# Performance work log

Hardware: AMD Instinct MI355X
Metric: run time of the kernel (lower is better)

## Reference

```python
import jax, jax.numpy as jnp
import numpy as np

P = 2    # padding
R = 2    # ref[0]: rows/cols gathered as conv channels
WP = 3   # ref[1]: conv kernel length along border


def setup_inputs() -> dict:
    key = jax.random.key(0)
    ks = jax.random.split(key, 8)
    B, C, H, W = 8, 128, 256, 256
    HID = 8
    x = jax.random.normal(ks[0], (B, C, H, W), dtype=jnp.float32)
    # stacked params for 4 border MLPs: order top, bottom, left, right
    w1 = jax.random.normal(ks[1], (4, HID, R, WP), dtype=jnp.float32) * 0.3
    b1 = jax.random.normal(ks[2], (4, HID), dtype=jnp.float32) * 0.1
    w2 = jax.random.normal(ks[3], (4, HID, HID), dtype=jnp.float32) * 0.3
    b2 = jax.random.normal(ks[4], (4, HID), dtype=jnp.float32) * 0.1
    w3 = jax.random.normal(ks[5], (4, 1, HID), dtype=jnp.float32) * 0.3
    b3 = jax.random.normal(ks[6], (4, 1), dtype=jnp.float32) * 0.1
    return {"x": x, "w1": w1, "b1": b1, "w2": w2, "b2": b2, "w3": w3, "b3": b3}


def _mlp(slab, w1, b1, w2, b2, w3, b3):
    # slab: (B, R, L, C) -- R gathered lines as channels, L border length, C image channels
    L = slab.shape[2]
    # valid conv along L with WP taps: windows (B, R, WP, L-WP+1, C)
    wins = jnp.stack([slab[:, :, k:L - WP + 1 + k, :] for k in range(WP)], axis=2)
    h = jax.nn.relu(jnp.einsum('brklc,hrk->bhlc', wins, w1) + b1[None, :, None, None])
    h = jax.nn.relu(jnp.einsum('bhlc,gh->bglc', h, w2) + b2[None, :, None, None])
    o = jax.nn.relu(jnp.einsum('bglc,og->bolc', h, w3) + b3[None, :, None, None])
    return o[:, 0]  # (B, L-2, C)


def reference(x, w1, b1, w2, b2, w3, b3):
    B, C, H, W = x.shape
    H2, W2 = H + 2 * P, W + 2 * P
    xp = jnp.zeros((B, C, H2, W2), x.dtype).at[:, :, P:H + P, P:W + P].set(x)
    for i in range(P):
        # top: gather rows [P-i, P-i+R), write row P-1-i, cols 1:W2-1
        top = _mlp(jnp.transpose(xp[:, :, P - i:P + R - i, :], (0, 2, 3, 1)),
                   w1[0], b1[0], w2[0], b2[0], w3[0], b3[0])  # (B, W2-2, C)
        xp = xp.at[:, :, P - 1 - i, 1:W2 - 1].set(jnp.transpose(top, (0, 2, 1)))
        # bottom
        bot = _mlp(jnp.transpose(xp[:, :, H2 - 1 - (R + P) + i:H2 - 1 - P + i, :], (0, 2, 3, 1)),
                   w1[1], b1[1], w2[1], b2[1], w3[1], b3[1])
        xp = xp.at[:, :, H + P + i, 1:W2 - 1].set(jnp.transpose(bot, (0, 2, 1)))
        # left: gather cols, transpose so cols act as channels
        lef = _mlp(jnp.transpose(xp[:, :, :, P - i:P + R - i], (0, 3, 2, 1)),
                   w1[2], b1[2], w2[2], b2[2], w3[2], b3[2])  # (B, H2-2, C)
        xp = xp.at[:, :, 1:H2 - 1, P - 1 - i].set(jnp.transpose(lef, (0, 2, 1)))
        # right
        rig = _mlp(jnp.transpose(xp[:, :, :, W2 - 1 - (R + P) + i:W2 - 1 - P + i], (0, 3, 2, 1)),
                   w1[3], b1[3], w2[3], b2[3], w3[3], b3[3])
        xp = xp.at[:, :, 1:H2 - 1, W + P + i].set(jnp.transpose(rig, (0, 2, 1)))
    return xp
```

## Files before the change

### kernel.cpp

```cpp
#include <hip/hip_runtime.h>


__device__ __forceinline__ int bmap(int r) { return r < 4 ? r : r - 251; }

__device__ __forceinline__ float mlp6(const float* __restrict__ v,
                                      const float* __restrict__ W1s,
                                      const float* __restrict__ B1s,
                                      const float* __restrict__ W2s,
                                      const float* __restrict__ B2s,
                                      const float* __restrict__ W3s,
                                      float b3s)
{
    float h1[8];
#pragma unroll
    for (int h = 0; h < 8; ++h) {
        float a = B1s[h];
#pragma unroll
        for (int q = 0; q < 6; ++q) a = fmaf(v[q], W1s[h * 6 + q], a);
        h1[h] = fmaxf(a, 0.f);
    }
    float h2[8];
#pragma unroll
    for (int g = 0; g < 8; ++g) {
        float a = B2s[g];
#pragma unroll
        for (int h = 0; h < 8; ++h) a = fmaf(h1[h], W2s[g * 8 + h], a);
        h2[g] = fmaxf(a, 0.f);
    }
    float o = b3s;
#pragma unroll
    for (int g = 0; g < 8; ++g) o = fmaf(h2[g], W3s[g], o);
    return fmaxf(o, 0.f);
}

__global__ __launch_bounds__(256) void border_kernel(
    const float* __restrict__ x,
    const float* __restrict__ w1, const float* __restrict__ b1,
    const float* __restrict__ w2, const float* __restrict__ b2,
    const float* __restrict__ w3, const float* __restrict__ b3,
    float* __restrict__ out)
{
    const int tid = threadIdx.x;
    const int bc  = blockIdx.x;
    const float* xs = x + (size_t)bc * 65536;
    float*       os = out + (size_t)bc * 67600;

    __shared__ float rowS[9][260];
    __shared__ float colS[9][260];
    __shared__ float W1[4][8][6];
    __shared__ float B1[4][8];
    __shared__ float W2[4][8][8];
    __shared__ float B2[4][8];
    __shared__ float W3[4][8];
    __shared__ float B3[4];

    for (int idx = tid; idx < 9 * 260; idx += 256) {
        (&rowS[0][0])[idx] = 0.f;
        (&colS[0][0])[idx] = 0.f;
    }
    for (int idx = tid; idx < 4 * 8 * 6; idx += 256) (&W1[0][0][0])[idx] = w1[idx];
    for (int idx = tid; idx < 4 * 8 * 8; idx += 256) (&W2[0][0][0])[idx] = w2[idx];
    if (tid < 32) {
        (&B1[0][0])[tid] = b1[tid];
        (&B2[0][0])[tid] = b2[tid];
        (&W3[0][0])[tid] = w3[tid];
    }
    if (tid < 4) B3[tid] = b3[tid];
    __syncthreads();

    for (int which = 0; which < 5; ++which) {
        int xr = which < 2 ? which : 251 + which;
        rowS[2 + which][2 + tid] = xs[xr * 256 + tid];
        colS[2 + which][2 + tid] = xs[tid * 256 + xr];
    }
    __syncthreads();

    for (int it = 0; it < 2; ++it) {
        for (int task = tid; task < 516; task += 256) {
            int s, j;
            int rin0, rin1, rout;
            if (task < 258) { s = 0; j = task + 1;       rin0 = 2 - it;   rin1 = 3 - it;   rout = 1 - it; }
            else            { s = 1; j = task - 258 + 1; rin0 = 255 + it; rin1 = 256 + it; rout = 258 + it; }
            int a0 = bmap(rin0), a1 = bmap(rin1);
            float v[6];
            v[0] = rowS[a0][j - 1]; v[1] = rowS[a0][j]; v[2] = rowS[a0][j + 1];
            v[3] = rowS[a1][j - 1]; v[4] = rowS[a1][j]; v[5] = rowS[a1][j + 1];
            float o = mlp6(v, &W1[s][0][0], B1[s], &W2[s][0][0], B2[s], W3[s], B3[s]);
            rowS[bmap(rout)][j] = o;
            if (j < 4 || j >= 255) colS[bmap(j)][rout] = o;
        }
        __syncthreads();
        for (int task = tid; task < 516; task += 256) {
            int s, r;
            int cin0, cin1, cout;
            if (task < 258) { s = 2; r = task + 1;       cin0 = 2 - it;   cin1 = 3 - it;   cout = 1 - it; }
            else            { s = 3; r = task - 258 + 1; cin0 = 255 + it; cin1 = 256 + it; cout = 258 + it; }
            int a0 = bmap(cin0), a1 = bmap(cin1);
            float v[6];
            v[0] = colS[a0][r - 1]; v[1] = colS[a0][r]; v[2] = colS[a0][r + 1];
            v[3] = colS[a1][r - 1]; v[4] = colS[a1][r]; v[5] = colS[a1][r + 1];
            float o = mlp6(v, &W1[s][0][0], B1[s], &W2[s][0][0], B2[s], W3[s], B3[s]);
            colS[bmap(cout)][r] = o;
            if (r < 4 || r >= 255) rowS[bmap(r)][cout] = o;
        }
        __syncthreads();
    }

    for (int idx = tid; idx < 4 * 260; idx += 256) {
        int w = idx / 260, cc = idx % 260;
        int rr = w < 2 ? w : 256 + w;
        os[(size_t)rr * 260 + cc] = rowS[bmap(rr)][cc];
    }
    for (int idx = tid; idx < 4 * 256; idx += 256) {
        int w = idx >> 8, r = (idx & 255) + 2;
        int cc = w < 2 ? w : 256 + w;
        os[(size_t)r * 260 + cc] = colS[bmap(cc)][r];
    }
}

__global__ __launch_bounds__(256) void copy_kernel(const float* __restrict__ x,
                                                   float* __restrict__ out)
{
    const int n2 = 8 * 128 * 256 * 128;
    int i = blockIdx.x * 256 + threadIdx.x;
    const int stride = gridDim.x * 256;
    for (; i < n2; i += stride) {
        int row = i >> 7;
        int pos = (i & 127) << 1;
        int bc  = row >> 8;
        int r   = row & 255;
        const float2 val = *(const float2*)(x + ((size_t)row << 8) + pos);
        *(float2*)(out + (size_t)bc * 67600 + (r + 2) * 260 + 2 + pos) = val;
    }
}

extern "C" void kernel_launch(void* const* d_in, const int* in_sizes, int n_in,
                              void* d_out, int out_size, void* d_ws, size_t ws_size,
                              hipStream_t stream)
{
    const float* x  = (const float*)d_in[0];
    const float* w1 = (const float*)d_in[1];
    const float* b1 = (const float*)d_in[2];
    const float* w2 = (const float*)d_in[3];
    const float* b2 = (const float*)d_in[4];
    const float* w3 = (const float*)d_in[5];
    const float* b3 = (const float*)d_in[6];
    float* out = (float*)d_out;

    copy_kernel<<<2048, 256, 0, stream>>>(x, out);
    border_kernel<<<1024, 256, 0, stream>>>(x, w1, b1, w2, b2, w3, b3, out);
}
```

Before: 140.8 us.

## Run border kernel first, then assemble interior rows with aligned float4 stores

The MLP weights are no longer staged in shared memory. Each border stage is templated on its MLP index so the compiler can turn the weights into uniform scalar loads. The kernels run in the opposite order: border_kernel writes the border first, then assemble_kernel writes every full output row with 16-byte-aligned float4 stores, reading back the border columns it overwrites. This is meant to replace the misaligned float2 interior stores with wider aligned ones, at the cost of extra reads of already-written border values and a dependency between the two kernels.

```diff
diff --git a/kernel.cpp b/kernel.cpp
--- a/kernel.cpp
+++ b/kernel.cpp
@@ -3,34 +3,86 @@
 
 __device__ __forceinline__ int bmap(int r) { return r < 4 ? r : r - 251; }
 
+template <int S>
 __device__ __forceinline__ float mlp6(const float* __restrict__ v,
-                                      const float* __restrict__ W1s,
-                                      const float* __restrict__ B1s,
-                                      const float* __restrict__ W2s,
-                                      const float* __restrict__ B2s,
-                                      const float* __restrict__ W3s,
-                                      float b3s)
+                                      const float* __restrict__ w1,
+                                      const float* __restrict__ b1,
+                                      const float* __restrict__ w2,
+                                      const float* __restrict__ b2,
+                                      const float* __restrict__ w3,
+                                      const float* __restrict__ b3)
 {
+    const float* __restrict__ W1 = w1 + S * 48;
+    const float* __restrict__ B1 = b1 + S * 8;
+    const float* __restrict__ W2 = w2 + S * 64;
+    const float* __restrict__ B2 = b2 + S * 8;
+    const float* __restrict__ W3 = w3 + S * 8;
+    const float  b3s = b3[S];
+
     float h1[8];
 #pragma unroll
     for (int h = 0; h < 8; ++h) {
-        float a = B1s[h];
+        float a = B1[h];
 #pragma unroll
-        for (int q = 0; q < 6; ++q) a = fmaf(v[q], W1s[h * 6 + q], a);
+        for (int q = 0; q < 6; ++q) a = fmaf(v[q], W1[h * 6 + q], a);
         h1[h] = fmaxf(a, 0.f);
     }
     float h2[8];
 #pragma unroll
     for (int g = 0; g < 8; ++g) {
-        float a = B2s[g];
+        float a = B2[g];
 #pragma unroll
-        for (int h = 0; h < 8; ++h) a = fmaf(h1[h], W2s[g * 8 + h], a);
+        for (int h = 0; h < 8; ++h) a = fmaf(h1[h], W2[g * 8 + h], a);
         h2[g] = fmaxf(a, 0.f);
     }
     float o = b3s;
 #pragma unroll
-    for (int g = 0; g < 8; ++g) o = fmaf(h2[g], W3s[g], o);
+    for (int g = 0; g < 8; ++g) o = fmaf(h2[g], W3[g], o);
     return fmaxf(o, 0.f);
+}
+
+template <int S>
+__device__ __forceinline__ void hstage(int it, int tid,
+                                       float (*rowS)[260], float (*colS)[260],
+                                       const float* __restrict__ w1, const float* __restrict__ b1,
+                                       const float* __restrict__ w2, const float* __restrict__ b2,
+                                       const float* __restrict__ w3, const float* __restrict__ b3)
+{
+    int rin0, rin1, rout;
+    if (S == 0) { rin0 = 2 - it;   rin1 = 3 - it;   rout = 1 - it;   }
+    else        { rin0 = 255 + it; rin1 = 256 + it; rout = 258 + it; }
+    const int a0 = bmap(rin0), a1 = bmap(rin1), ao = bmap(rout);
+    for (int j0 = tid; j0 < 258; j0 += 256) {
+        int j = j0 + 1;
+        float v[6];
+        v[0] = rowS[a0][j - 1]; v[1] = rowS[a0][j]; v[2] = rowS[a0][j + 1];
+        v[3] = rowS[a1][j - 1]; v[4] = rowS[a1][j]; v[5] = rowS[a1][j + 1];
+        float o = mlp6<S>(v, w1, b1, w2, b2, w3, b3);
+        rowS[ao][j] = o;
+        if (j < 4 || j >= 255) colS[bmap(j)][rout] = o;
+    }
+}
+
+template <int S>
+__device__ __forceinline__ void vstage(int it, int tid,
+                                       float (*rowS)[260], float (*colS)[260],
+                                       const float* __restrict__ w1, const float* __restrict__ b1,
+                                       const float* __restrict__ w2, const float* __restrict__ b2,
+                                       const float* __restrict__ w3, const float* __restrict__ b3)
+{
+    int cin0, cin1, cout;
+    if (S == 2) { cin0 = 2 - it;   cin1 = 3 - it;   cout = 1 - it;   }
+    else        { cin0 = 255 + it; cin1 = 256 + it; cout = 258 + it; }
+    const int a0 = bmap(cin0), a1 = bmap(cin1), ao = bmap(cout);
+    for (int r0 = tid; r0 < 258; r0 += 256) {
+        int r = r0 + 1;
+        float v[6];
+        v[0] = colS[a0][r - 1]; v[1] = colS[a0][r]; v[2] = colS[a0][r + 1];
+        v[3] = colS[a1][r - 1]; v[4] = colS[a1][r]; v[5] = colS[a1][r + 1];
+        float o = mlp6<S>(v, w1, b1, w2, b2, w3, b3);
+        colS[ao][r] = o;
+        if (r < 4 || r >= 255) rowS[bmap(r)][cout] = o;
+    }
 }
 
 __global__ __launch_bounds__(256) void border_kernel(
@@ -47,25 +99,11 @@
 
     __shared__ float rowS[9][260];
     __shared__ float colS[9][260];
-    __shared__ float W1[4][8][6];
-    __shared__ float B1[4][8];
-    __shared__ float W2[4][8][8];
-    __shared__ float B2[4][8];
-    __shared__ float W3[4][8];
-    __shared__ float B3[4];
 
     for (int idx = tid; idx < 9 * 260; idx += 256) {
         (&rowS[0][0])[idx] = 0.f;
         (&colS[0][0])[idx] = 0.f;
     }
-    for (int idx = tid; idx < 4 * 8 * 6; idx += 256) (&W1[0][0][0])[idx] = w1[idx];
-    for (int idx = tid; idx < 4 * 8 * 8; idx += 256) (&W2[0][0][0])[idx] = w2[idx];
-    if (tid < 32) {
-        (&B1[0][0])[tid] = b1[tid];
-        (&B2[0][0])[tid] = b2[tid];
-        (&W3[0][0])[tid] = w3[tid];
-    }
-    if (tid < 4) B3[tid] = b3[tid];
     __syncthreads();
 
     for (int which = 0; which < 5; ++which) {
@@ -76,33 +114,11 @@
     __syncthreads();
 
     for (int it = 0; it < 2; ++it) {
-        for (int task = tid; task < 516; task += 256) {
-            int s, j;
-            int rin0, rin1, rout;
-            if (task < 258) { s = 0; j = task + 1;       rin0 = 2 - it;   rin1 = 3 - it;   rout = 1 - it; }
-            else            { s = 1; j = task - 258 + 1; rin0 = 255 + it; rin1 = 256 + it; rout = 258 + it; }
-            int a0 = bmap(rin0), a1 = bmap(rin1);
-            float v[6];
-            v[0] = rowS[a0][j - 1]; v[1] = rowS[a0][j]; v[2] = rowS[a0][j + 1];
-            v[3] = rowS[a1][j - 1]; v[4] = rowS[a1][j]; v[5] = rowS[a1][j + 1];
-            float o = mlp6(v, &W1[s][0][0], B1[s], &W2[s][0][0], B2[s], W3[s], B3[s]);
-            rowS[bmap(rout)][j] = o;
-            if (j < 4 || j >= 255) colS[bmap(j)][rout] = o;
-        }
+        hstage<0>(it, tid, rowS, colS, w1, b1, w2, b2, w3, b3);
+        hstage<1>(it, tid, rowS, colS, w1, b1, w2, b2, w3, b3);
         __syncthreads();
-        for (int task = tid; task < 516; task += 256) {
-            int s, r;
-            int cin0, cin1, cout;
-            if (task < 258) { s = 2; r = task + 1;       cin0 = 2 - it;   cin1 = 3 - it;   cout = 1 - it; }
-            else            { s = 3; r = task - 258 + 1; cin0 = 255 + it; cin1 = 256 + it; cout = 258 + it; }
-            int a0 = bmap(cin0), a1 = bmap(cin1);
-            float v[6];
-            v[0] = colS[a0][r - 1]; v[1] = colS[a0][r]; v[2] = colS[a0][r + 1];
-            v[3] = colS[a1][r - 1]; v[4] = colS[a1][r]; v[5] = colS[a1][r + 1];
-            float o = mlp6(v, &W1[s][0][0], B1[s], &W2[s][0][0], B2[s], W3[s], B3[s]);
-            colS[bmap(cout)][r] = o;
-            if (r < 4 || r >= 255) rowS[bmap(r)][cout] = o;
-        }
+        vstage<2>(it, tid, rowS, colS, w1, b1, w2, b2, w3, b3);
+        vstage<3>(it, tid, rowS, colS, w1, b1, w2, b2, w3, b3);
         __syncthreads();
     }
 
@@ -118,20 +134,35 @@
     }
 }
 
-__global__ __launch_bounds__(256) void copy_kernel(const float* __restrict__ x,
-                                                   float* __restrict__ out)
+__global__ __launch_bounds__(256) void assemble_kernel(const float* __restrict__ x,
+                                                       float* out)
 {
-    const int n2 = 8 * 128 * 256 * 128;
-    int i = blockIdx.x * 256 + threadIdx.x;
-    const int stride = gridDim.x * 256;
-    for (; i < n2; i += stride) {
-        int row = i >> 7;
-        int pos = (i & 127) << 1;
-        int bc  = row >> 8;
-        int r   = row & 255;
-        const float2 val = *(const float2*)(x + ((size_t)row << 8) + pos);
-        *(float2*)(out + (size_t)bc * 67600 + (r + 2) * 260 + 2 + pos) = val;
+    const int bc = blockIdx.y;
+    const float* xrowbase = x + (size_t)bc * 65536;
+    float*       os       = out + (size_t)bc * 67600;
+
+    int idx = blockIdx.x * 256 + threadIdx.x;
+    int r   = idx / 65;
+    int k   = idx - r * 65;
+
+    float*       orow = os + (size_t)(r + 2) * 260;
+    const float* xrow = xrowbase + (size_t)r * 256;
+
+    float4 val;
+    if (k == 0) {
+        float2 b = *(const float2*)(orow);
+        float2 a = *(const float2*)(xrow);
+        val = make_float4(b.x, b.y, a.x, a.y);
+    } else if (k == 64) {
+        float2 a = *(const float2*)(xrow + 254);
+        float2 b = *(const float2*)(orow + 258);
+        val = make_float4(a.x, a.y, b.x, b.y);
+    } else {
+        float2 a = *(const float2*)(xrow + 4 * k - 2);
+        float2 c = *(const float2*)(xrow + 4 * k);
+        val = make_float4(a.x, a.y, c.x, c.y);
     }
+    *(float4*)(orow + 4 * k) = val;
 }
 
 extern "C" void kernel_launch(void* const* d_in, const int* in_sizes, int n_in,
@@ -147,6 +178,6 @@
     const float* b3 = (const float*)d_in[6];
     float* out = (float*)d_out;
 
-    copy_kernel<<<2048, 256, 0, stream>>>(x, out);
     border_kernel<<<1024, 256, 0, stream>>>(x, w1, b1, w2, b2, w3, b3, out);
+    assemble_kernel<<<dim3(65, 1024), 256, 0, stream>>>(x, out);
 }
```

After: 147.0 us. 1.04x slower.
